# Optimization experiments

Hardware: AMD Instinct MI355X
Metric: run time of the kernel (lower is better)

## Reference

```python
import jax, jax.numpy as jnp
import numpy as np

EPS = 1e-5
DIL = 1
PAD = 1
STRIDE = 1

def conv2d(x, w, stride=1, pad=1, dil=1):
    return jax.lax.conv_general_dilated(x, w, (stride, stride), [(pad, pad), (pad, pad)],
                                        rhs_dilation=(dil, dil),
                                        dimension_numbers=('NCHW', 'OIHW', 'NCHW'))

def batchnorm(x, g, b, m, v):
    inv = g / jnp.sqrt(v + EPS)
    return x * inv[None, :, None, None] + (b - m * inv)[None, :, None, None]

def _bilinear(img, y, x):
    # img: [C,H,W]; y,x: [Ho,Wo] float sample coords; zero padding outside.
    H, W = img.shape[1], img.shape[2]
    y0 = jnp.floor(y); x0 = jnp.floor(x)
    ty = y - y0; tx = x - x0
    y0i = y0.astype(jnp.int32); x0i = x0.astype(jnp.int32)
    def g(yi, xi):
        valid = (yi >= 0) & (yi < H) & (xi >= 0) & (xi < W)
        v = img[:, jnp.clip(yi, 0, H - 1), jnp.clip(xi, 0, W - 1)]  # [C,Ho,Wo]
        return jnp.where(valid[None], v, jnp.zeros((), img.dtype))
    return (g(y0i, x0i) * ((1 - ty) * (1 - tx))[None]
            + g(y0i, x0i + 1) * ((1 - ty) * tx)[None]
            + g(y0i + 1, x0i) * (ty * (1 - tx))[None]
            + g(y0i + 1, x0i + 1) * (ty * tx)[None])

def deform_conv(x, w, offset, stride=1, pad=1, dil=1):
    # offset: [B, 18, Ho, Wo], channels 0:9 = dy per kernel tap (row-major), 9:18 = dx.
    B, C, H, W = x.shape
    Co = w.shape[0]
    Ho = (H + 2 * pad - dil * 2 - 1) // stride + 1
    Wo = (W + 2 * pad - dil * 2 - 1) // stride + 1
    off = offset.reshape(B, 2, 9, Ho, Wo)
    iy = (jnp.arange(Ho) * stride - pad).astype(x.dtype)
    ix = (jnp.arange(Wo) * stride - pad).astype(x.dtype)
    wk = w.reshape(Co, C, 9)
    out = jnp.zeros((B, Co, Ho, Wo), x.dtype)
    for k in range(9):  # fixed 3x3 kernel taps
        ky, kx = k // 3, k % 3
        ys = iy[:, None] + ky * dil + off[:, 0, k]  # [B,Ho,Wo]
        xs = ix[None, :] + kx * dil + off[:, 1, k]
        val = jax.vmap(_bilinear)(x, ys, xs)        # [B,C,Ho,Wo]
        out = out + jnp.einsum('bchw,oc->bohw', val, wk[:, :, k])
    return out

def offset_bias(dil, dtype):
    bw = jnp.array([[-1., 0., 1.]] * 3, dtype) * (dil - 1)
    bh = bw.T
    return jnp.concatenate([bh.reshape(-1), bw.reshape(-1)])  # [18]

def setup_inputs() -> dict:
    key = jax.random.key(0)
    ks = jax.random.split(key, 12)
    B, C, H, W = 8, 256, 56, 56
    inp = {
        'x': jax.random.normal(ks[0], (B, C, H, W), jnp.float32),
        'conv1_w': jax.random.normal(ks[1], (C, C, 3, 3), jnp.float32) * 0.02,
        'bn1_g': jax.random.normal(ks[2], (C,), jnp.float32) * 0.1 + 1.0,
        'bn1_b': jax.random.normal(ks[3], (C,), jnp.float32) * 0.1,
        'bn1_m': jax.random.normal(ks[4], (C,), jnp.float32) * 0.1,
        'bn1_v': jax.random.uniform(ks[5], (C,), jnp.float32) + 0.5,
        'off_w': jax.random.normal(ks[6], (18, C, 3, 3), jnp.float32) * 0.01,
        'off_b': jnp.zeros((18,), jnp.float32),
        'conv2_w': jax.random.normal(ks[7], (C, C, 3, 3), jnp.float32) * 0.02,
        'bn2_g': jax.random.normal(ks[8], (C,), jnp.float32) * 0.1 + 1.0,
        'bn2_b': jax.random.normal(ks[9], (C,), jnp.float32) * 0.1,
        'bn2_m': jax.random.normal(ks[10], (C,), jnp.float32) * 0.1,
        'bn2_v': jax.random.uniform(ks[11], (C,), jnp.float32) + 0.5,
    }
    return inp

def reference(x, conv1_w, bn1_g, bn1_b, bn1_m, bn1_v, off_w, off_b, conv2_w, bn2_g, bn2_b, bn2_m, bn2_v):
    residual = x
    out = conv2d(x, conv1_w, STRIDE, PAD, DIL)
    out = jax.nn.relu(batchnorm(out, bn1_g, bn1_b, bn1_m, bn1_v))
    offset = conv2d(out, off_w, STRIDE, PAD, DIL) + off_b[None, :, None, None]
    offset = offset + offset_bias(DIL, out.dtype)[None, :, None, None]
    out = deform_conv(out, conv2_w, offset, STRIDE, PAD, DIL)
    out = batchnorm(out, bn2_g, bn2_b, bn2_m, bn2_v)
    return jax.nn.relu(out + residual)
```

## Files before the change

kernel.cpp:

```cpp
#include <hip/hip_runtime.h>

#define NB 8
#define NH 56
#define NW 56
#define NHW 3136
#define NCHW 802816
#define NPIX 25088
#define NHP 58
#define EPSV 1e-5f
#define BUFS 20480

typedef float f32x4 __attribute__((ext_vector_type(4)));
typedef __bf16 bf16x8 __attribute__((ext_vector_type(8)));

__device__ __forceinline__ unsigned short f2b(float f) {
  unsigned int u = __float_as_uint(f);
  u += 0x7FFFu + ((u >> 16) & 1u);
  return (unsigned short)(u >> 16);
}
__device__ __forceinline__ float blo(unsigned int u){ return __uint_as_float(u << 16); }
__device__ __forceinline__ float bhi(unsigned int u){ return __uint_as_float(u & 0xFFFF0000u); }
__device__ __forceinline__ unsigned int pack_trunc(float f0, float f1) {
  return __builtin_amdgcn_perm(__float_as_uint(f1), __float_as_uint(f0), 0x07060302u);
}
__device__ __forceinline__ void soft_barrier() {
  __builtin_amdgcn_s_waitcnt(0xC07F);
  __builtin_amdgcn_s_barrier();
}

__global__ __launch_bounds__(256) void clear_borders(
    unsigned short* __restrict__ xbp, unsigned short* __restrict__ t1b)
{
  int i = blockIdx.x*256 + threadIdx.x;
  int q = i & 31; int pid = i >> 5;
  int b = pid / 228, j = pid % 228;
  int y, x;
  if (j < 58)       { y = 0;  x = j; }
  else if (j < 116) { y = 57; x = j - 58; }
  else { int jj = j - 116; y = 1 + (jj >> 1); x = (jj & 1) * 57; }
  size_t addr = ((size_t)(b*NHP + y)*NHP + x)*256 + q*8;
  uint4 z = make_uint4(0u,0u,0u,0u);
  *(uint4*)(xbp + addr) = z;
  *(uint4*)(t1b + addr) = z;
}

__global__ __launch_bounds__(256) void prep_x(
    const float* __restrict__ x, unsigned short* __restrict__ xbp)
{
  __shared__ float T[64][65];
  const int pxt  = blockIdx.x * 64;
  const int cg   = blockIdx.y * 64;
  const int b    = pxt / NHW;
  const int rem0 = pxt % NHW;
  const int t    = threadIdx.x;
  const int pl   = t & 63;
  const int c0   = t >> 6;
  const float* src = x + (size_t)b*NCHW + rem0;
  #pragma unroll
  for (int it = 0; it < 16; ++it) {
    int c = c0 + it*4;
    T[c][pl] = src[(size_t)(cg + c)*NHW + pl];
  }
  __syncthreads();
  const int pr = t >> 5;
  const int cp = t & 31;
  #pragma unroll
  for (int it = 0; it < 8; ++it) {
    int pxl = pr + it*8;
    int rem = rem0 + pxl;
    int ho = rem / NW, wo = rem % NW;
    unsigned int pk = ((unsigned int)f2b(T[cp*2+1][pxl]) << 16) | (unsigned int)f2b(T[cp*2][pxl]);
    *(unsigned int*)(xbp + ((size_t)(b*NHP + ho + 1)*NHP + (wo + 1))*256 + cg + cp*2) = pk;
  }
}

__global__ __launch_bounds__(256) void prep_w(
    const float* __restrict__ w, unsigned short* __restrict__ wp)
{
  int i = blockIdx.x*256 + threadIdx.x;
  int co = i / 2304;
  int r  = i % 2304;
  int k  = r >> 8;
  int ci = r & 255;
  wp[i] = f2b(w[((size_t)co*256 + ci)*9 + k]);
}

__global__ __launch_bounds__(256) void prep_w3(
    const float* __restrict__ ow, unsigned short* __restrict__ w3p)
{
  int i = blockIdx.x*256 + threadIdx.x;
  int co = i / 2304;
  int r  = i % 2304;
  int k  = r >> 8;
  int ci = r & 255;
  w3p[i] = (co < 18) ? f2b(ow[((size_t)co*256 + ci)*9 + k]) : (unsigned short)0;
}

__global__ __launch_bounds__(512, 4) void gemm_conv1(
    const unsigned short* __restrict__ xbp, const unsigned short* __restrict__ w1p,
    const float* __restrict__ gam, const float* __restrict__ bet,
    const float* __restrict__ mu,  const float* __restrict__ var,
    unsigned short* __restrict__ t1b)
{
  __shared__ unsigned short SMEM[2*BUFS];

  const int bx   = blockIdx.x;
  const int nbx  = (bx & 7)*49 + (bx >> 3);
  const int m0   = nbx * 64;
  const int t    = threadIdx.x;
  const int lane = t & 63;
  const int wv   = t >> 6;
  const int wvM  = wv & 1;
  const int wvN  = wv >> 1;
  const int quad = lane >> 4;
  const int l15  = lane & 15;

  const int srow = t >> 3;
  const int seg  = t & 7;
  const int sxor = srow & 7;
  const int px  = m0 + srow;
  const int b   = px / NHW, rem = px % NHW;
  const int ho  = rem / NW, wo = rem % NW;
  const unsigned int pbase = ((unsigned int)(b*NHP + ho)*NHP + wo)*256u + seg*8u;

  f32x4 acc[2][4];
  #pragma unroll
  for (int i = 0; i < 2; ++i)
    #pragma unroll
    for (int j = 0; j < 4; ++j) acc[i][j] = (f32x4)(0.f);

  uint4 pA, pB0, pB1, pB2, pB3;
  {
    pA  = *(const uint4*)(xbp + pbase);
    const unsigned int rb = seg*8u;
    pB0 = *(const uint4*)(w1p + (size_t)(srow      )*2304 + rb);
    pB1 = *(const uint4*)(w1p + (size_t)(srow +  64)*2304 + rb);
    pB2 = *(const uint4*)(w1p + (size_t)(srow + 128)*2304 + rb);
    pB3 = *(const uint4*)(w1p + (size_t)(srow + 192)*2304 + rb);
    *(uint4*)(&SMEM[srow*64 + ((seg ^ sxor)*8)]) = pA;
    *(uint4*)(&SMEM[4096 + (srow      )*64 + ((seg ^ sxor)*8)]) = pB0;
    *(uint4*)(&SMEM[4096 + (srow +  64)*64 + ((seg ^ sxor)*8)]) = pB1;
    *(uint4*)(&SMEM[4096 + (srow + 128)*64 + ((seg ^ sxor)*8)]) = pB2;
    *(uint4*)(&SMEM[4096 + (srow + 192)*64 + ((seg ^ sxor)*8)]) = pB3;
    pA  = *(const uint4*)(xbp + pbase + 64u);
    const unsigned int rb1 = 64u + seg*8u;
    pB0 = *(const uint4*)(w1p + (size_t)(srow      )*2304 + rb1);
    pB1 = *(const uint4*)(w1p + (size_t)(srow +  64)*2304 + rb1);
    pB2 = *(const uint4*)(w1p + (size_t)(srow + 128)*2304 + rb1);
    pB3 = *(const uint4*)(w1p + (size_t)(srow + 192)*2304 + rb1);
    soft_barrier();
  }

  for (int r = 0; r < 36; ++r) {
    unsigned short* Ac = SMEM + (r & 1)*BUFS;
    unsigned short* Bc = Ac + 4096;
    unsigned short* An = SMEM + ((r + 1) & 1)*BUFS;
    unsigned short* Bn = An + 4096;
    *(uint4*)(&An[srow*64 + ((seg ^ sxor)*8)]) = pA;
    *(uint4*)(&Bn[(srow      )*64 + ((seg ^ sxor)*8)]) = pB0;
    *(uint4*)(&Bn[(srow +  64)*64 + ((seg ^ sxor)*8)]) = pB1;
    *(uint4*)(&Bn[(srow + 128)*64 + ((seg ^ sxor)*8)]) = pB2;
    *(uint4*)(&Bn[(srow + 192)*64 + ((seg ^ sxor)*8)]) = pB3;
    {
      const int rn = (r < 34) ? r + 2 : 35;
      const int kn = rn >> 2, cicn = rn & 3;
      const int kyn = kn/3, kxn = kn - kyn*3;
      pA  = *(const uint4*)(xbp + pbase + (unsigned int)((kyn*NHP + kxn)*256 + cicn*64));
      const unsigned int rb = (unsigned int)(rn*64) + seg*8u;
      pB0 = *(const uint4*)(w1p + (size_t)(srow      )*2304 + rb);
      pB1 = *(const uint4*)(w1p + (size_t)(srow +  64)*2304 + rb);
      pB2 = *(const uint4*)(w1p + (size_t)(srow + 128)*2304 + rb);
      pB3 = *(const uint4*)(w1p + (size_t)(srow + 192)*2304 + rb);
    }
    #pragma unroll
    for (int kk = 0; kk < 2; ++kk) {
      const int s8 = (kk*4 + quad) ^ (l15 & 7);
      bf16x8 af[2], bfr[4];
      #pragma unroll
      for (int mt = 0; mt < 2; ++mt)
        af[mt] = *(const bf16x8*)(&Ac[(wvM*32 + mt*16 + l15)*64 + s8*8]);
      #pragma unroll
      for (int nt = 0; nt < 4; ++nt)
        bfr[nt] = *(const bf16x8*)(&Bc[(wvN*64 + nt*16 + l15)*64 + s8*8]);
      #pragma unroll
      for (int mt = 0; mt < 2; ++mt)
        #pragma unroll
        for (int nt = 0; nt < 4; ++nt)
          acc[mt][nt] = __builtin_amdgcn_mfma_f32_16x16x32_bf16(af[mt], bfr[nt], acc[mt][nt], 0, 0, 0);
    }
    soft_barrier();
  }

  __syncthreads();
  unsigned short* Sw = SMEM + wv*2304;
  #pragma unroll
  for (int nt = 0; nt < 4; ++nt) {
    const int co = wvN*64 + nt*16 + l15;
    const float inv  = gam[co] * rsqrtf(var[co] + EPSV);
    const float beta = bet[co] - mu[co]*inv;
    #pragma unroll
    for (int mt = 0; mt < 2; ++mt) {
      #pragma unroll
      for (int rr = 0; rr < 4; ++rr) {
        const int pxl = mt*16 + quad*4 + rr;
        float val = acc[mt][nt][rr]*inv + beta;
        val = val > 0.f ? val : 0.f;
        Sw[pxl*72 + nt*16 + l15] = f2b(val);
      }
    }
  }
  #pragma unroll
  for (int i = 0; i < 4; ++i) {
    const int pxl = (lane >> 3) + 8*i;
    const int sc  = lane & 7;
    uint4 q = *(const uint4*)(&Sw[pxl*72 + sc*8]);
    const int pg = m0 + wvM*32 + pxl;
    const int bb = pg / NHW, rm = pg % NHW;
    const int hh = rm / NW, ww = rm % NW;
    *(uint4*)(t1b + ((size_t)(bb*NHP + hh + 1)*NHP + ww + 1)*256 + wvN*64 + sc*8) = q;
  }
}

__global__ __launch_bounds__(256, 8) void gemm_off(
    const unsigned short* __restrict__ t1b, const unsigned short* __restrict__ w3p,
    const float* __restrict__ ob, float* __restrict__ toff)
{
  __shared__ unsigned short Al[4096];
  __shared__ unsigned short Bl[2048];

  const int bx  = blockIdx.x;
  const int nbx = (bx & 7)*49 + (bx >> 3);
  const int m0  = nbx * 64;
  const int kc = blockIdx.y;
  const int t    = threadIdx.x;
  const int lane = t & 63;
  const int wv   = t >> 6;
  const int quad = lane >> 4;
  const int l15  = lane & 15;

  const int arow = t >> 2;
  const int as4  = t & 3;
  const int axor = arow & 7;
  const int pxa  = m0 + arow;
  const int ba   = pxa / NHW, rema = pxa % NHW;
  const unsigned int pbase = ((unsigned int)(ba*NHP + rema/NW)*NHP + rema%NW)*256u;

  const int brow = t >> 3;
  const int bs   = t & 7;

  f32x4 acc[2];
  #pragma unroll
  for (int nt = 0; nt < 2; ++nt) {
    float init = 0.f;
    if (kc == 0) { int co = nt*16 + l15; init = (co < 18) ? ob[co] : 0.f; }
    acc[nt] = (f32x4)(init);
  }

  uint4 pA0, pA1, pB;
  {
    const int r = kc*9, k = r >> 2, cic = r & 3;
    const int ky = k/3, kx = k - ky*3;
    const unsigned int base = pbase + (unsigned int)((ky*NHP + kx)*256 + cic*64);
    pA0 = *(const uint4*)(t1b + base + as4*8);
    pA1 = *(const uint4*)(t1b + base + (as4+4)*8);
    pB  = *(const uint4*)(w3p + (size_t)brow*2304 + r*64 + bs*8);
  }

  for (int rr = 0; rr < 9; ++rr) {
    const int r = kc*9 + rr;
    __syncthreads();
    *(uint4*)(&Al[arow*64 + ((as4     ^ axor)*8)]) = pA0;
    *(uint4*)(&Al[arow*64 + (((as4+4) ^ axor)*8)]) = pA1;
    *(uint4*)(&Bl[brow*64 + ((bs ^ (brow & 7))*8)]) = pB;
    {
      const int rn = (rr < 8) ? r + 1 : r;
      const int kn = rn >> 2, cicn = rn & 3;
      const int kyn = kn/3, kxn = kn - kyn*3;
      const unsigned int base = pbase + (unsigned int)((kyn*NHP + kxn)*256 + cicn*64);
      pA0 = *(const uint4*)(t1b + base + as4*8);
      pA1 = *(const uint4*)(t1b + base + (as4+4)*8);
      pB  = *(const uint4*)(w3p + (size_t)brow*2304 + rn*64 + bs*8);
    }
    soft_barrier();
    #pragma unroll
    for (int kk = 0; kk < 2; ++kk) {
      const int s8 = (kk*4 + quad) ^ (l15 & 7);
      bf16x8 af = *(const bf16x8*)(&Al[(wv*16 + l15)*64 + s8*8]);
      #pragma unroll
      for (int nt = 0; nt < 2; ++nt) {
        bf16x8 bfr = *(const bf16x8*)(&Bl[(nt*16 + l15)*64 + s8*8]);
        acc[nt] = __builtin_amdgcn_mfma_f32_16x16x32_bf16(af, bfr, acc[nt], 0, 0, 0);
      }
    }
  }
  #pragma unroll
  for (int nt = 0; nt < 2; ++nt) {
    const int co = nt*16 + l15;
    if (co < 18) {
      #pragma unroll
      for (int rr2 = 0; rr2 < 4; ++rr2) {
        const int pg = m0 + wv*16 + quad*4 + rr2;
        const int bb = pg / NHW, rm = pg % NHW;
        atomicAdd(&toff[(size_t)bb*(18*NHW) + (size_t)co*NHW + rm], acc[nt][rr2]);
      }
    }
  }
}

__global__ __launch_bounds__(512, 4) void gemm_deform(
    const unsigned short* __restrict__ t1b, const unsigned short* __restrict__ w2p,
    const float* __restrict__ toff, const float* __restrict__ xres,
    const float* __restrict__ gam, const float* __restrict__ bet,
    const float* __restrict__ mu,  const float* __restrict__ var,
    float* __restrict__ outp)
{
  __shared__ unsigned short SMEM[2*BUFS];

  const int bid  = blockIdx.x;
  const int nb   = (bid & 7)*49 + (bid >> 3);
  const int m0   = nb * 64;
  const int t    = threadIdx.x;
  const int lane = t & 63;
  const int wv   = t >> 6;
  const int wvM  = wv & 1;
  const int wvN  = wv >> 1;
  const int quad = lane >> 4;
  const int l15  = lane & 15;

  const int srow = t >> 3;
  const int seg  = t & 7;
  const int sxor = srow & 7;
  const int px   = m0 + srow;
  const int b    = px / NHW, rem = px % NHW;
  const int ho   = rem / NW, wo = rem % NW;
  const int obb  = b*(18*NHW) + rem;
  const unsigned int prowb = (unsigned int)(b*NHP);

  f32x4 acc[2][4];
  #pragma unroll
  for (int i = 0; i < 2; ++i)
    #pragma unroll
    for (int j = 0; j < 4; ++j) acc[i][j] = (f32x4)(0.f);

  unsigned int o00, o01, o10, o11;
  float w00, w01, w10, w11;
#define COORDS(KK) {                                                   \
    const int ky_ = (KK)/3, kx_ = (KK) - ky_*3;                        \
    const float offy = toff[obb + (KK)*NHW];                           \
    const float offx = toff[obb + (9+(KK))*NHW];                       \
    const float yf = (float)(ho - 1 + ky_) + offy;                     \
    const float xf = (float)(wo - 1 + kx_) + offx;                     \
    const float y0f = floorf(yf), x0f = floorf(xf);                    \
    const float ty = yf - y0f,   tx = xf - x0f;                        \
    const int y0p = (int)y0f + 1, x0p = (int)x0f + 1;                  \
    const int cy0 = min(max(y0p,   0), NHP-1);                         \
    const int cy1 = min(max(y0p+1, 0), NHP-1);                         \
    const int cx0 = min(max(x0p,   0), NHP-1);                         \
    const int cx1 = min(max(x0p+1, 0), NHP-1);                         \
    w00 = (1.f-ty)*(1.f-tx);  w01 = (1.f-ty)*tx;                       \
    w10 = ty*(1.f-tx);        w11 = ty*tx;                             \
    o00 = ((prowb + cy0)*NHP + cx0)*256u + seg*8u;                     \
    o01 = ((prowb + cy0)*NHP + cx1)*256u + seg*8u;                     \
    o10 = ((prowb + cy1)*NHP + cx0)*256u + seg*8u;                     \
    o11 = ((prowb + cy1)*NHP + cx1)*256u + seg*8u;                     \
  }

#define PACK_WRITE(DST) {                                                        \
    uint4 res;                                                                   \
    { float a0 = w00*blo(pc00.x) + w01*blo(pc01.x) + w10*blo(pc10.x) + w11*blo(pc11.x); \
      float a1 = w00*bhi(pc00.x) + w01*bhi(pc01.x) + w10*bhi(pc10.x) + w11*bhi(pc11.x); \
      res.x = pack_trunc(a0, a1); }                                              \
    { float a0 = w00*blo(pc00.y) + w01*blo(pc01.y) + w10*blo(pc10.y) + w11*blo(pc11.y); \
      float a1 = w00*bhi(pc00.y) + w01*bhi(pc01.y) + w10*bhi(pc10.y) + w11*bhi(pc11.y); \
      res.y = pack_trunc(a0, a1); }                                              \
    { float a0 = w00*blo(pc00.z) + w01*blo(pc01.z) + w10*blo(pc10.z) + w11*blo(pc11.z); \
      float a1 = w00*bhi(pc00.z) + w01*bhi(pc01.z) + w10*bhi(pc10.z) + w11*bhi(pc11.z); \
      res.z = pack_trunc(a0, a1); }                                              \
    { float a0 = w00*blo(pc00.w) + w01*blo(pc01.w) + w10*blo(pc10.w) + w11*blo(pc11.w); \
      float a1 = w00*bhi(pc00.w) + w01*bhi(pc01.w) + w10*bhi(pc10.w) + w11*bhi(pc11.w); \
      res.w = pack_trunc(a0, a1); }                                              \
    *(uint4*)(&(DST)[srow*64 + ((seg ^ sxor)*8)]) = res;                         \
  }

  COORDS(0);
  uint4 pc00, pc01, pc10, pc11, pB0, pB1, pB2, pB3;
  {
    pc00 = *(const uint4*)(t1b + o00);
    pc01 = *(const uint4*)(t1b + o01);
    pc10 = *(const uint4*)(t1b + o10);
    pc11 = *(const uint4*)(t1b + o11);
    const unsigned int rb = seg*8u;
    pB0 = *(const uint4*)(w2p + (size_t)(srow      )*2304 + rb);
    pB1 = *(const uint4*)(w2p + (size_t)(srow +  64)*2304 + rb);
    pB2 = *(const uint4*)(w2p + (size_t)(srow + 128)*2304 + rb);
    pB3 = *(const uint4*)(w2p + (size_t)(srow + 192)*2304 + rb);
    PACK_WRITE(SMEM);
    *(uint4*)(&SMEM[4096 + (srow      )*64 + ((seg ^ sxor)*8)]) = pB0;
    *(uint4*)(&SMEM[4096 + (srow +  64)*64 + ((seg ^ sxor)*8)]) = pB1;
    *(uint4*)(&SMEM[4096 + (srow + 128)*64 + ((seg ^ sxor)*8)]) = pB2;
    *(uint4*)(&SMEM[4096 + (srow + 192)*64 + ((seg ^ sxor)*8)]) = pB3;
    pc00 = *(const uint4*)(t1b + o00 + 64u);
    pc01 = *(const uint4*)(t1b + o01 + 64u);
    pc10 = *(const uint4*)(t1b + o10 + 64u);
    pc11 = *(const uint4*)(t1b + o11 + 64u);
    const unsigned int rb1 = 64u + seg*8u;
    pB0 = *(const uint4*)(w2p + (size_t)(srow      )*2304 + rb1);
    pB1 = *(const uint4*)(w2p + (size_t)(srow +  64)*2304 + rb1);
    pB2 = *(const uint4*)(w2p + (size_t)(srow + 128)*2304 + rb1);
    pB3 = *(const uint4*)(w2p + (size_t)(srow + 192)*2304 + rb1);
    soft_barrier();
  }

  for (int r = 0; r < 36; ++r) {
    unsigned short* Ac = SMEM + (r & 1)*BUFS;
    unsigned short* Bc = Ac + 4096;
    unsigned short* An = SMEM + ((r + 1) & 1)*BUFS;
    unsigned short* Bn = An + 4096;
    PACK_WRITE(An);
    *(uint4*)(&Bn[(srow      )*64 + ((seg ^ sxor)*8)]) = pB0;
    *(uint4*)(&Bn[(srow +  64)*64 + ((seg ^ sxor)*8)]) = pB1;
    *(uint4*)(&Bn[(srow + 128)*64 + ((seg ^ sxor)*8)]) = pB2;
    *(uint4*)(&Bn[(srow + 192)*64 + ((seg ^ sxor)*8)]) = pB3;
    if ((r & 3) == 2 && r < 34) COORDS((r + 2) >> 2);
    {
      const int rn = (r < 34) ? r + 2 : 35;
      const unsigned int cio = (unsigned int)((rn & 3)*64);
      pc00 = *(const uint4*)(t1b + o00 + cio);
      pc01 = *(const uint4*)(t1b + o01 + cio);
      pc10 = *(const uint4*)(t1b + o10 + cio);
      pc11 = *(const uint4*)(t1b + o11 + cio);
      const unsigned int rb = (unsigned int)(rn*64) + seg*8u;
      pB0 = *(const uint4*)(w2p + (size_t)(srow      )*2304 + rb);
      pB1 = *(const uint4*)(w2p + (size_t)(srow +  64)*2304 + rb);
      pB2 = *(const uint4*)(w2p + (size_t)(srow + 128)*2304 + rb);
      pB3 = *(const uint4*)(w2p + (size_t)(srow + 192)*2304 + rb);
    }
    #pragma unroll
    for (int kk = 0; kk < 2; ++kk) {
      const int s8 = (kk*4 + quad) ^ (l15 & 7);
      bf16x8 af[2], bfr[4];
      #pragma unroll
      for (int mt = 0; mt < 2; ++mt)
        af[mt] = *(const bf16x8*)(&Ac[(wvM*32 + mt*16 + l15)*64 + s8*8]);
      #pragma unroll
      for (int nt = 0; nt < 4; ++nt)
        bfr[nt] = *(const bf16x8*)(&Bc[(wvN*64 + nt*16 + l15)*64 + s8*8]);
      #pragma unroll
      for (int mt = 0; mt < 2; ++mt)
        #pragma unroll
        for (int nt = 0; nt < 4; ++nt)
          acc[mt][nt] = __builtin_amdgcn_mfma_f32_16x16x32_bf16(af[mt], bfr[nt], acc[mt][nt], 0, 0, 0);
    }
    soft_barrier();
  }
#undef COORDS
#undef PACK_WRITE

  __syncthreads();
  float* Sl = (float*)SMEM + wv*1056;
  const int pxl_r = lane & 31;
  const int csel  = lane >> 5;
  const int pg    = m0 + wvM*32 + pxl_r;
  const int bo    = pg / NHW, remo = pg % NHW;
  const size_t obase = (size_t)bo*NCHW + remo;
  #pragma unroll
  for (int h = 0; h < 2; ++h) {
    #pragma unroll
    for (int nt2 = 0; nt2 < 2; ++nt2) {
      const int nt = h*2 + nt2;
      #pragma unroll
      for (int mt = 0; mt < 2; ++mt) {
        #pragma unroll
        for (int rr = 0; rr < 4; ++rr) {
          const int pxl = mt*16 + quad*4 + rr;
          Sl[pxl*33 + nt2*16 + l15] = acc[mt][nt][rr];
        }
      }
    }
    #pragma unroll
    for (int j = 0; j < 16; ++j) {
      const int col = csel*16 + j;
      const int co  = wvN*64 + h*32 + col;
      const float inv  = gam[co] * rsqrtf(var[co] + EPSV);
      const float beta = bet[co] - mu[co]*inv;
      const size_t off = obase + (size_t)co*NHW;
      float val = Sl[pxl_r*33 + col];
      float o = val*inv + beta + xres[off];
      outp[off] = o > 0.f ? o : 0.f;
    }
  }
}

extern "C" void kernel_launch(void* const* d_in, const int* in_sizes, int n_in,
                              void* d_out, int out_size, void* d_ws, size_t ws_size,
                              hipStream_t stream) {
  const float* x   = (const float*)d_in[0];
  const float* w1  = (const float*)d_in[1];
  const float* g1  = (const float*)d_in[2];
  const float* b1  = (const float*)d_in[3];
  const float* m1  = (const float*)d_in[4];
  const float* v1  = (const float*)d_in[5];
  const float* ow  = (const float*)d_in[6];
  const float* ob  = (const float*)d_in[7];
  const float* w2  = (const float*)d_in[8];
  const float* g2  = (const float*)d_in[9];
  const float* b2  = (const float*)d_in[10];
  const float* m2  = (const float*)d_in[11];
  const float* v2  = (const float*)d_in[12];
  float* out = (float*)d_out;

  const size_t PADSZ = (size_t)NB*NHP*NHP*256;
  unsigned short* xbp = (unsigned short*)d_ws;
  unsigned short* t1b = xbp + PADSZ;
  float*          tof = (float*)(t1b + PADSZ);
  unsigned short* w1p = (unsigned short*)(tof + (size_t)NB*18*NHW);
  unsigned short* w2p = w1p + (size_t)589824;
  unsigned short* w3p = w2p + (size_t)589824;

  clear_borders<<<228, 256, 0, stream>>>(xbp, t1b);
  dim3 gp(392, 4, 1);
  prep_x<<<gp, 256, 0, stream>>>(x, xbp);
  prep_w<<<2304, 256, 0, stream>>>(w1, w1p);
  prep_w<<<2304, 256, 0, stream>>>(w2, w2p);
  prep_w3<<<288, 256, 0, stream>>>(ow, w3p);
  hipMemsetAsync(tof, 0, (size_t)NB*18*NHW*sizeof(float), stream);

  gemm_conv1<<<392, 512, 0, stream>>>(xbp, w1p, g1, b1, m1, v1, t1b);
  dim3 go(392, 4, 1);
  gemm_off<<<go, 256, 0, stream>>>(t1b, w3p, ob, tof);
  gemm_deform<<<392, 512, 0, stream>>>(t1b, w2p, tof, x, g2, b2, m2, v2, out);
}
```

Measured before the change: 250.7 us.

## Deepen register prefetch to three stages and move LDS stores after MFMA

Both GEMM main loops (conv1 and the deformable conv2) now keep two sets of prefetch registers and issue global loads three rounds ahead instead of two. The loop is unrolled by two so the register sets alternate. The shared-memory stores for the next round are moved to after the MFMA block, so global-load latency has more time to hide behind compute. In the deformable loop the bilinear weights are snapshotted per stage and COORDS is computed one round earlier. The cost is higher register pressure, which may reduce occupancy or cause spills.

```diff
diff --git a/kernel.cpp b/kernel.cpp
--- a/kernel.cpp
+++ b/kernel.cpp
@@ -129,67 +129,71 @@
     #pragma unroll
     for (int j = 0; j < 4; ++j) acc[i][j] = (f32x4)(0.f);
 
-  uint4 pA, pB0, pB1, pB2, pB3;
+  uint4 saA, saB0, saB1, saB2, saB3;
+  uint4 sbA, sbB0, sbB1, sbB2, sbB3;
+
+#define C1_ISSUE(SA_, SB0_, SB1_, SB2_, SB3_, RN) {                       \
+    const int kn_ = (RN) >> 2, cicn_ = (RN) & 3;                          \
+    const int kyn_ = kn_/3, kxn_ = kn_ - kyn_*3;                          \
+    SA_  = *(const uint4*)(xbp + pbase + (unsigned int)((kyn_*NHP + kxn_)*256 + cicn_*64)); \
+    const unsigned int rb_ = (unsigned int)((RN)*64) + seg*8u;            \
+    SB0_ = *(const uint4*)(w1p + (size_t)(srow      )*2304 + rb_);        \
+    SB1_ = *(const uint4*)(w1p + (size_t)(srow +  64)*2304 + rb_);        \
+    SB2_ = *(const uint4*)(w1p + (size_t)(srow + 128)*2304 + rb_);        \
+    SB3_ = *(const uint4*)(w1p + (size_t)(srow + 192)*2304 + rb_);        \
+  }
+
   {
-    pA  = *(const uint4*)(xbp + pbase);
-    const unsigned int rb = seg*8u;
-    pB0 = *(const uint4*)(w1p + (size_t)(srow      )*2304 + rb);
-    pB1 = *(const uint4*)(w1p + (size_t)(srow +  64)*2304 + rb);
-    pB2 = *(const uint4*)(w1p + (size_t)(srow + 128)*2304 + rb);
-    pB3 = *(const uint4*)(w1p + (size_t)(srow + 192)*2304 + rb);
-    *(uint4*)(&SMEM[srow*64 + ((seg ^ sxor)*8)]) = pA;
-    *(uint4*)(&SMEM[4096 + (srow      )*64 + ((seg ^ sxor)*8)]) = pB0;
-    *(uint4*)(&SMEM[4096 + (srow +  64)*64 + ((seg ^ sxor)*8)]) = pB1;
-    *(uint4*)(&SMEM[4096 + (srow + 128)*64 + ((seg ^ sxor)*8)]) = pB2;
-    *(uint4*)(&SMEM[4096 + (srow + 192)*64 + ((seg ^ sxor)*8)]) = pB3;
-    pA  = *(const uint4*)(xbp + pbase + 64u);
-    const unsigned int rb1 = 64u + seg*8u;
-    pB0 = *(const uint4*)(w1p + (size_t)(srow      )*2304 + rb1);
-    pB1 = *(const uint4*)(w1p + (size_t)(srow +  64)*2304 + rb1);
-    pB2 = *(const uint4*)(w1p + (size_t)(srow + 128)*2304 + rb1);
-    pB3 = *(const uint4*)(w1p + (size_t)(srow + 192)*2304 + rb1);
+    uint4 tA, tB0, tB1, tB2, tB3;
+    C1_ISSUE(tA, tB0, tB1, tB2, tB3, 0);
+    *(uint4*)(&SMEM[srow*64 + ((seg ^ sxor)*8)]) = tA;
+    *(uint4*)(&SMEM[4096 + (srow      )*64 + ((seg ^ sxor)*8)]) = tB0;
+    *(uint4*)(&SMEM[4096 + (srow +  64)*64 + ((seg ^ sxor)*8)]) = tB1;
+    *(uint4*)(&SMEM[4096 + (srow + 128)*64 + ((seg ^ sxor)*8)]) = tB2;
+    *(uint4*)(&SMEM[4096 + (srow + 192)*64 + ((seg ^ sxor)*8)]) = tB3;
+    C1_ISSUE(sbA, sbB0, sbB1, sbB2, sbB3, 1);
+    C1_ISSUE(saA, saB0, saB1, saB2, saB3, 2);
     soft_barrier();
   }
 
-  for (int r = 0; r < 36; ++r) {
-    unsigned short* Ac = SMEM + (r & 1)*BUFS;
-    unsigned short* Bc = Ac + 4096;
-    unsigned short* An = SMEM + ((r + 1) & 1)*BUFS;
-    unsigned short* Bn = An + 4096;
-    *(uint4*)(&An[srow*64 + ((seg ^ sxor)*8)]) = pA;
-    *(uint4*)(&Bn[(srow      )*64 + ((seg ^ sxor)*8)]) = pB0;
-    *(uint4*)(&Bn[(srow +  64)*64 + ((seg ^ sxor)*8)]) = pB1;
-    *(uint4*)(&Bn[(srow + 128)*64 + ((seg ^ sxor)*8)]) = pB2;
-    *(uint4*)(&Bn[(srow + 192)*64 + ((seg ^ sxor)*8)]) = pB3;
-    {
-      const int rn = (r < 34) ? r + 2 : 35;
-      const int kn = rn >> 2, cicn = rn & 3;
-      const int kyn = kn/3, kxn = kn - kyn*3;
-      pA  = *(const uint4*)(xbp + pbase + (unsigned int)((kyn*NHP + kxn)*256 + cicn*64));
-      const unsigned int rb = (unsigned int)(rn*64) + seg*8u;
-      pB0 = *(const uint4*)(w1p + (size_t)(srow      )*2304 + rb);
-      pB1 = *(const uint4*)(w1p + (size_t)(srow +  64)*2304 + rb);
-      pB2 = *(const uint4*)(w1p + (size_t)(srow + 128)*2304 + rb);
-      pB3 = *(const uint4*)(w1p + (size_t)(srow + 192)*2304 + rb);
-    }
-    #pragma unroll
-    for (int kk = 0; kk < 2; ++kk) {
-      const int s8 = (kk*4 + quad) ^ (l15 & 7);
-      bf16x8 af[2], bfr[4];
-      #pragma unroll
-      for (int mt = 0; mt < 2; ++mt)
-        af[mt] = *(const bf16x8*)(&Ac[(wvM*32 + mt*16 + l15)*64 + s8*8]);
-      #pragma unroll
-      for (int nt = 0; nt < 4; ++nt)
-        bfr[nt] = *(const bf16x8*)(&Bc[(wvN*64 + nt*16 + l15)*64 + s8*8]);
-      #pragma unroll
-      for (int mt = 0; mt < 2; ++mt)
-        #pragma unroll
-        for (int nt = 0; nt < 4; ++nt)
-          acc[mt][nt] = __builtin_amdgcn_mfma_f32_16x16x32_bf16(af[mt], bfr[nt], acc[mt][nt], 0, 0, 0);
-    }
-    soft_barrier();
-  }
+#define C1_ROUND(R, SA_, SB0_, SB1_, SB2_, SB3_) {                        \
+    const int r_ = (R);                                                   \
+    unsigned short* Ac = SMEM + (r_ & 1)*BUFS;                            \
+    unsigned short* Bc = Ac + 4096;                                       \
+    unsigned short* An = SMEM + ((r_ + 1) & 1)*BUFS;                      \
+    unsigned short* Bn = An + 4096;                                       \
+    _Pragma("unroll")                                                     \
+    for (int kk = 0; kk < 2; ++kk) {                                      \
+      const int s8 = (kk*4 + quad) ^ (l15 & 7);                           \
+      bf16x8 af[2], bfr[4];                                               \
+      _Pragma("unroll")                                                   \
+      for (int mt = 0; mt < 2; ++mt)                                      \
+        af[mt] = *(const bf16x8*)(&Ac[(wvM*32 + mt*16 + l15)*64 + s8*8]); \
+      _Pragma("unroll")                                                   \
+      for (int nt = 0; nt < 4; ++nt)                                      \
+        bfr[nt] = *(const bf16x8*)(&Bc[(wvN*64 + nt*16 + l15)*64 + s8*8]);\
+      _Pragma("unroll")                                                   \
+      for (int mt = 0; mt < 2; ++mt)                                      \
+        _Pragma("unroll")                                                 \
+        for (int nt = 0; nt < 4; ++nt)                                    \
+          acc[mt][nt] = __builtin_amdgcn_mfma_f32_16x16x32_bf16(af[mt], bfr[nt], acc[mt][nt], 0, 0, 0); \
+    }                                                                     \
+    *(uint4*)(&An[srow*64 + ((seg ^ sxor)*8)]) = SA_;                     \
+    *(uint4*)(&Bn[(srow      )*64 + ((seg ^ sxor)*8)]) = SB0_;            \
+    *(uint4*)(&Bn[(srow +  64)*64 + ((seg ^ sxor)*8)]) = SB1_;            \
+    *(uint4*)(&Bn[(srow + 128)*64 + ((seg ^ sxor)*8)]) = SB2_;            \
+    *(uint4*)(&Bn[(srow + 192)*64 + ((seg ^ sxor)*8)]) = SB3_;            \
+    const int rn_ = (r_ < 33) ? r_ + 3 : 35;                              \
+    C1_ISSUE(SA_, SB0_, SB1_, SB2_, SB3_, rn_);                           \
+    soft_barrier();                                                       \
+  }
+
+  for (int r = 0; r < 36; r += 2) {
+    C1_ROUND(r,     sbA, sbB0, sbB1, sbB2, sbB3);
+    C1_ROUND(r + 1, saA, saB0, saB1, saB2, saB3);
+  }
+#undef C1_ROUND
+#undef C1_ISSUE
 
   __syncthreads();
   unsigned short* Sw = SMEM + wv*2304;
@@ -365,96 +369,107 @@
     o11 = ((prowb + cy1)*NHP + cx1)*256u + seg*8u;                     \
   }
 
-#define PACK_WRITE(DST) {                                                        \
-    uint4 res;                                                                   \
-    { float a0 = w00*blo(pc00.x) + w01*blo(pc01.x) + w10*blo(pc10.x) + w11*blo(pc11.x); \
-      float a1 = w00*bhi(pc00.x) + w01*bhi(pc01.x) + w10*bhi(pc10.x) + w11*bhi(pc11.x); \
-      res.x = pack_trunc(a0, a1); }                                              \
-    { float a0 = w00*blo(pc00.y) + w01*blo(pc01.y) + w10*blo(pc10.y) + w11*blo(pc11.y); \
-      float a1 = w00*bhi(pc00.y) + w01*bhi(pc01.y) + w10*bhi(pc10.y) + w11*bhi(pc11.y); \
-      res.y = pack_trunc(a0, a1); }                                              \
-    { float a0 = w00*blo(pc00.z) + w01*blo(pc01.z) + w10*blo(pc10.z) + w11*blo(pc11.z); \
-      float a1 = w00*bhi(pc00.z) + w01*bhi(pc01.z) + w10*bhi(pc10.z) + w11*bhi(pc11.z); \
-      res.z = pack_trunc(a0, a1); }                                              \
-    { float a0 = w00*blo(pc00.w) + w01*blo(pc01.w) + w10*blo(pc10.w) + w11*blo(pc11.w); \
-      float a1 = w00*bhi(pc00.w) + w01*bhi(pc01.w) + w10*bhi(pc10.w) + w11*bhi(pc11.w); \
-      res.w = pack_trunc(a0, a1); }                                              \
-    *(uint4*)(&(DST)[srow*64 + ((seg ^ sxor)*8)]) = res;                         \
-  }
+#define PACKW(C00,C01,C10,C11,W00,W01,W10,W11,DST) {                            \
+    uint4 res;                                                                  \
+    { float a0 = W00*blo(C00.x) + W01*blo(C01.x) + W10*blo(C10.x) + W11*blo(C11.x); \
+      float a1 = W00*bhi(C00.x) + W01*bhi(C01.x) + W10*bhi(C10.x) + W11*bhi(C11.x); \
+      res.x = pack_trunc(a0, a1); }                                             \
+    { float a0 = W00*blo(C00.y) + W01*blo(C01.y) + W10*blo(C10.y) + W11*blo(C11.y); \
+      float a1 = W00*bhi(C00.y) + W01*bhi(C01.y) + W10*bhi(C10.y) + W11*bhi(C11.y); \
+      res.y = pack_trunc(a0, a1); }                                             \
+    { float a0 = W00*blo(C00.z) + W01*blo(C01.z) + W10*blo(C10.z) + W11*blo(C11.z); \
+      float a1 = W00*bhi(C00.z) + W01*bhi(C01.z) + W10*bhi(C10.z) + W11*bhi(C11.z); \
+      res.z = pack_trunc(a0, a1); }                                             \
+    { float a0 = W00*blo(C00.w) + W01*blo(C01.w) + W10*blo(C10.w) + W11*blo(C11.w); \
+      float a1 = W00*bhi(C00.w) + W01*bhi(C01.w) + W10*bhi(C10.w) + W11*bhi(C11.w); \
+      res.w = pack_trunc(a0, a1); }                                             \
+    *(uint4*)(&(DST)[srow*64 + ((seg ^ sxor)*8)]) = res;                        \
+  }
+
+#define ISSUEC(C00,C01,C10,C11,W00,W01,W10,W11,RN) {                            \
+    const unsigned int cio_ = (unsigned int)(((RN) & 3)*64);                    \
+    C00 = *(const uint4*)(t1b + o00 + cio_);                                    \
+    C01 = *(const uint4*)(t1b + o01 + cio_);                                    \
+    C10 = *(const uint4*)(t1b + o10 + cio_);                                    \
+    C11 = *(const uint4*)(t1b + o11 + cio_);                                    \
+    W00 = w00; W01 = w01; W10 = w10; W11 = w11;                                 \
+  }
+
+#define ISSUEB(RN) {                                                            \
+    const unsigned int rb_ = (unsigned int)((RN)*64) + seg*8u;                  \
+    pB0 = *(const uint4*)(w2p + (size_t)(srow      )*2304 + rb_);               \
+    pB1 = *(const uint4*)(w2p + (size_t)(srow +  64)*2304 + rb_);               \
+    pB2 = *(const uint4*)(w2p + (size_t)(srow + 128)*2304 + rb_);               \
+    pB3 = *(const uint4*)(w2p + (size_t)(srow + 192)*2304 + rb_);               \
+  }
+
+  uint4 ca00, ca01, ca10, ca11, cb00, cb01, cb10, cb11;
+  float cwa00, cwa01, cwa10, cwa11, cwb00, cwb01, cwb10, cwb11;
+  uint4 pB0, pB1, pB2, pB3;
 
   COORDS(0);
-  uint4 pc00, pc01, pc10, pc11, pB0, pB1, pB2, pB3;
   {
-    pc00 = *(const uint4*)(t1b + o00);
-    pc01 = *(const uint4*)(t1b + o01);
-    pc10 = *(const uint4*)(t1b + o10);
-    pc11 = *(const uint4*)(t1b + o11);
-    const unsigned int rb = seg*8u;
-    pB0 = *(const uint4*)(w2p + (size_t)(srow      )*2304 + rb);
-    pB1 = *(const uint4*)(w2p + (size_t)(srow +  64)*2304 + rb);
-    pB2 = *(const uint4*)(w2p + (size_t)(srow + 128)*2304 + rb);
-    pB3 = *(const uint4*)(w2p + (size_t)(srow + 192)*2304 + rb);
-    PACK_WRITE(SMEM);
+    uint4 t00, t01, t10, t11;
+    t00 = *(const uint4*)(t1b + o00);
+    t01 = *(const uint4*)(t1b + o01);
+    t10 = *(const uint4*)(t1b + o10);
+    t11 = *(const uint4*)(t1b + o11);
+    ISSUEB(0);
+    PACKW(t00, t01, t10, t11, w00, w01, w10, w11, SMEM);
     *(uint4*)(&SMEM[4096 + (srow      )*64 + ((seg ^ sxor)*8)]) = pB0;
     *(uint4*)(&SMEM[4096 + (srow +  64)*64 + ((seg ^ sxor)*8)]) = pB1;
     *(uint4*)(&SMEM[4096 + (srow + 128)*64 + ((seg ^ sxor)*8)]) = pB2;
     *(uint4*)(&SMEM[4096 + (srow + 192)*64 + ((seg ^ sxor)*8)]) = pB3;
-    pc00 = *(const uint4*)(t1b + o00 + 64u);
-    pc01 = *(const uint4*)(t1b + o01 + 64u);
-    pc10 = *(const uint4*)(t1b + o10 + 64u);
-    pc11 = *(const uint4*)(t1b + o11 + 64u);
-    const unsigned int rb1 = 64u + seg*8u;
-    pB0 = *(const uint4*)(w2p + (size_t)(srow      )*2304 + rb1);
-    pB1 = *(const uint4*)(w2p + (size_t)(srow +  64)*2304 + rb1);
-    pB2 = *(const uint4*)(w2p + (size_t)(srow + 128)*2304 + rb1);
-    pB3 = *(const uint4*)(w2p + (size_t)(srow + 192)*2304 + rb1);
+    ISSUEC(cb00, cb01, cb10, cb11, cwb00, cwb01, cwb10, cwb11, 1);
+    ISSUEB(1);
+    ISSUEC(ca00, ca01, ca10, ca11, cwa00, cwa01, cwa10, cwa11, 2);
     soft_barrier();
   }
 
-  for (int r = 0; r < 36; ++r) {
-    unsigned short* Ac = SMEM + (r & 1)*BUFS;
-    unsigned short* Bc = Ac + 4096;
-    unsigned short* An = SMEM + ((r + 1) & 1)*BUFS;
-    unsigned short* Bn = An + 4096;
-    PACK_WRITE(An);
-    *(uint4*)(&Bn[(srow      )*64 + ((seg ^ sxor)*8)]) = pB0;
-    *(uint4*)(&Bn[(srow +  64)*64 + ((seg ^ sxor)*8)]) = pB1;
-    *(uint4*)(&Bn[(srow + 128)*64 + ((seg ^ sxor)*8)]) = pB2;
-    *(uint4*)(&Bn[(srow + 192)*64 + ((seg ^ sxor)*8)]) = pB3;
-    if ((r & 3) == 2 && r < 34) COORDS((r + 2) >> 2);
-    {
-      const int rn = (r < 34) ? r + 2 : 35;
-      const unsigned int cio = (unsigned int)((rn & 3)*64);
-      pc00 = *(const uint4*)(t1b + o00 + cio);
-      pc01 = *(const uint4*)(t1b + o01 + cio);
-      pc10 = *(const uint4*)(t1b + o10 + cio);
-      pc11 = *(const uint4*)(t1b + o11 + cio);
-      const unsigned int rb = (unsigned int)(rn*64) + seg*8u;
-      pB0 = *(const uint4*)(w2p + (size_t)(srow      )*2304 + rb);
-      pB1 = *(const uint4*)(w2p + (size_t)(srow +  64)*2304 + rb);
-      pB2 = *(const uint4*)(w2p + (size_t)(srow + 128)*2304 + rb);
-      pB3 = *(const uint4*)(w2p + (size_t)(srow + 192)*2304 + rb);
-    }
-    #pragma unroll
-    for (int kk = 0; kk < 2; ++kk) {
-      const int s8 = (kk*4 + quad) ^ (l15 & 7);
-      bf16x8 af[2], bfr[4];
-      #pragma unroll
-      for (int mt = 0; mt < 2; ++mt)
-        af[mt] = *(const bf16x8*)(&Ac[(wvM*32 + mt*16 + l15)*64 + s8*8]);
-      #pragma unroll
-      for (int nt = 0; nt < 4; ++nt)
-        bfr[nt] = *(const bf16x8*)(&Bc[(wvN*64 + nt*16 + l15)*64 + s8*8]);
-      #pragma unroll
-      for (int mt = 0; mt < 2; ++mt)
-        #pragma unroll
-        for (int nt = 0; nt < 4; ++nt)
-          acc[mt][nt] = __builtin_amdgcn_mfma_f32_16x16x32_bf16(af[mt], bfr[nt], acc[mt][nt], 0, 0, 0);
-    }
-    soft_barrier();
-  }
+#define DROUND(R, C00,C01,C10,C11, W00,W01,W10,W11) {                           \
+    const int r_ = (R);                                                         \
+    unsigned short* Ac = SMEM + (r_ & 1)*BUFS;                                  \
+    unsigned short* Bc = Ac + 4096;                                             \
+    unsigned short* An = SMEM + ((r_ + 1) & 1)*BUFS;                            \
+    unsigned short* Bn = An + 4096;                                             \
+    if ((r_ & 3) == 1 && r_ < 33) COORDS((r_ + 3) >> 2);                        \
+    _Pragma("unroll")                                                           \
+    for (int kk = 0; kk < 2; ++kk) {                                            \
+      const int s8 = (kk*4 + quad) ^ (l15 & 7);                                 \
+      bf16x8 af[2], bfr[4];                                                     \
+      _Pragma("unroll")                                                         \
+      for (int mt = 0; mt < 2; ++mt)                                            \
+        af[mt] = *(const bf16x8*)(&Ac[(wvM*32 + mt*16 + l15)*64 + s8*8]);       \
+      _Pragma("unroll")                                                         \
+      for (int nt = 0; nt < 4; ++nt)                                            \
+        bfr[nt] = *(const bf16x8*)(&Bc[(wvN*64 + nt*16 + l15)*64 + s8*8]);      \
+      _Pragma("unroll")                                                         \
+      for (int mt = 0; mt < 2; ++mt)                                            \
+        _Pragma("unroll")                                                       \
+        for (int nt = 0; nt < 4; ++nt)                                          \
+          acc[mt][nt] = __builtin_amdgcn_mfma_f32_16x16x32_bf16(af[mt], bfr[nt], acc[mt][nt], 0, 0, 0); \
+    }                                                                           \
+    PACKW(C00, C01, C10, C11, W00, W01, W10, W11, An);                          \
+    *(uint4*)(&Bn[(srow      )*64 + ((seg ^ sxor)*8)]) = pB0;                   \
+    *(uint4*)(&Bn[(srow +  64)*64 + ((seg ^ sxor)*8)]) = pB1;                   \
+    *(uint4*)(&Bn[(srow + 128)*64 + ((seg ^ sxor)*8)]) = pB2;                   \
+    *(uint4*)(&Bn[(srow + 192)*64 + ((seg ^ sxor)*8)]) = pB3;                   \
+    const int rnB_ = (r_ < 34) ? r_ + 2 : 35;                                   \
+    ISSUEB(rnB_);                                                               \
+    const int rn3_ = (r_ < 33) ? r_ + 3 : 35;                                   \
+    ISSUEC(C00, C01, C10, C11, W00, W01, W10, W11, rn3_);                       \
+    soft_barrier();                                                             \
+  }
+
+  for (int r = 0; r < 36; r += 2) {
+    DROUND(r,     cb00, cb01, cb10, cb11, cwb00, cwb01, cwb10, cwb11);
+    DROUND(r + 1, ca00, ca01, ca10, ca11, cwa00, cwa01, cwa10, cwa11);
+  }
+#undef DROUND
+#undef ISSUEB
+#undef ISSUEC
+#undef PACKW
 #undef COORDS
-#undef PACK_WRITE
 
   __syncthreads();
   float* Sl = (float*)SMEM + wv*1056;
```

New measurement: 281.9 us. +12.4%, slower.

## Use direct global-to-LDS loads in conv GEMMs and merge prep launches

Applied to the files above, without the earlier changes.

Replaces the register-staged global loads and LDS stores for the A/B tiles in gemm_conv1, and for the weight tiles in gemm_deform, with global_load_lds DMA. This shortens prefetch distance to one stage and swaps the soft barrier for __syncthreads. It also folds the three weight-prep kernels into one launch and moves the offset-buffer memset into clear_borders. The intent is to cut VGPR pressure, LDS store instructions and launch overhead. The risk is that the shorter prefetch exposes memory latency, and the swizzle mapping for the DMA layout must match the existing reads.

```diff
diff --git a/kernel.cpp b/kernel.cpp
--- a/kernel.cpp
+++ b/kernel.cpp
@@ -9,6 +9,7 @@
 #define NHP 58
 #define EPSV 1e-5f
 #define BUFS 20480
+#define TOFN 451584
 
 typedef float f32x4 __attribute__((ext_vector_type(4)));
 typedef __bf16 bf16x8 __attribute__((ext_vector_type(8)));
@@ -27,9 +28,16 @@
   __builtin_amdgcn_s_waitcnt(0xC07F);
   __builtin_amdgcn_s_barrier();
 }
+__device__ __forceinline__ void dma16(const unsigned short* g, unsigned short* l) {
+  __builtin_amdgcn_global_load_lds(
+      (const __attribute__((address_space(1))) unsigned int*)g,
+      (__attribute__((address_space(3))) unsigned int*)l,
+      16, 0, 0);
+}
 
 __global__ __launch_bounds__(256) void clear_borders(
-    unsigned short* __restrict__ xbp, unsigned short* __restrict__ t1b)
+    unsigned short* __restrict__ xbp, unsigned short* __restrict__ t1b,
+    float* __restrict__ tof)
 {
   int i = blockIdx.x*256 + threadIdx.x;
   int q = i & 31; int pid = i >> 5;
@@ -42,6 +50,11 @@
   uint4 z = make_uint4(0u,0u,0u,0u);
   *(uint4*)(xbp + addr) = z;
   *(uint4*)(t1b + addr) = z;
+  int zi = i*8;
+  if (zi < TOFN) {
+    *(float4*)(tof + zi)     = make_float4(0.f,0.f,0.f,0.f);
+    *(float4*)(tof + zi + 4) = make_float4(0.f,0.f,0.f,0.f);
+  }
 }
 
 __global__ __launch_bounds__(256) void prep_x(
@@ -74,26 +87,25 @@
   }
 }
 
-__global__ __launch_bounds__(256) void prep_w(
-    const float* __restrict__ w, unsigned short* __restrict__ wp)
+__global__ __launch_bounds__(256) void prep_w_all(
+    const float* __restrict__ w1, const float* __restrict__ w2,
+    const float* __restrict__ ow,
+    unsigned short* __restrict__ w1p, unsigned short* __restrict__ w2p,
+    unsigned short* __restrict__ w3p)
 {
   int i = blockIdx.x*256 + threadIdx.x;
-  int co = i / 2304;
-  int r  = i % 2304;
-  int k  = r >> 8;
-  int ci = r & 255;
-  wp[i] = f2b(w[((size_t)co*256 + ci)*9 + k]);
-}
-
-__global__ __launch_bounds__(256) void prep_w3(
-    const float* __restrict__ ow, unsigned short* __restrict__ w3p)
-{
-  int i = blockIdx.x*256 + threadIdx.x;
-  int co = i / 2304;
-  int r  = i % 2304;
-  int k  = r >> 8;
-  int ci = r & 255;
-  w3p[i] = (co < 18) ? f2b(ow[((size_t)co*256 + ci)*9 + k]) : (unsigned short)0;
+  if (i < 589824) {
+    int co = i / 2304, r = i % 2304, k = r >> 8, ci = r & 255;
+    w1p[i] = f2b(w1[((size_t)co*256 + ci)*9 + k]);
+  } else if (i < 1179648) {
+    int j = i - 589824;
+    int co = j / 2304, r = j % 2304, k = r >> 8, ci = r & 255;
+    w2p[j] = f2b(w2[((size_t)co*256 + ci)*9 + k]);
+  } else {
+    int j = i - 1179648;
+    int co = j / 2304, r = j % 2304, k = r >> 8, ci = r & 255;
+    w3p[j] = (co < 18) ? f2b(ow[((size_t)co*256 + ci)*9 + k]) : (unsigned short)0;
+  }
 }
 
 __global__ __launch_bounds__(512, 4) void gemm_conv1(
@@ -117,11 +129,14 @@
 
   const int srow = t >> 3;
   const int seg  = t & 7;
-  const int sxor = srow & 7;
+  const int swz8 = ((seg ^ (srow & 7))*8);
   const int px  = m0 + srow;
   const int b   = px / NHW, rem = px % NHW;
   const int ho  = rem / NW, wo = rem % NW;
-  const unsigned int pbase = ((unsigned int)(b*NHP + ho)*NHP + wo)*256u + seg*8u;
+  const unsigned int pbaseA = ((unsigned int)(b*NHP + ho)*NHP + wo)*256u + (unsigned int)swz8;
+  const int rowB0 = wv*32 + (lane >> 3);
+  const unsigned int bswz = (unsigned int)(((lane & 7) ^ (lane >> 3))*8);
+  const int chA = wv*512;
 
   f32x4 acc[2][4];
   #pragma unroll
@@ -129,26 +144,12 @@
     #pragma unroll
     for (int j = 0; j < 4; ++j) acc[i][j] = (f32x4)(0.f);
 
-  uint4 pA, pB0, pB1, pB2, pB3;
   {
-    pA  = *(const uint4*)(xbp + pbase);
-    const unsigned int rb = seg*8u;
-    pB0 = *(const uint4*)(w1p + (size_t)(srow      )*2304 + rb);
-    pB1 = *(const uint4*)(w1p + (size_t)(srow +  64)*2304 + rb);
-    pB2 = *(const uint4*)(w1p + (size_t)(srow + 128)*2304 + rb);
-    pB3 = *(const uint4*)(w1p + (size_t)(srow + 192)*2304 + rb);
-    *(uint4*)(&SMEM[srow*64 + ((seg ^ sxor)*8)]) = pA;
-    *(uint4*)(&SMEM[4096 + (srow      )*64 + ((seg ^ sxor)*8)]) = pB0;
-    *(uint4*)(&SMEM[4096 + (srow +  64)*64 + ((seg ^ sxor)*8)]) = pB1;
-    *(uint4*)(&SMEM[4096 + (srow + 128)*64 + ((seg ^ sxor)*8)]) = pB2;
-    *(uint4*)(&SMEM[4096 + (srow + 192)*64 + ((seg ^ sxor)*8)]) = pB3;
-    pA  = *(const uint4*)(xbp + pbase + 64u);
-    const unsigned int rb1 = 64u + seg*8u;
-    pB0 = *(const uint4*)(w1p + (size_t)(srow      )*2304 + rb1);
-    pB1 = *(const uint4*)(w1p + (size_t)(srow +  64)*2304 + rb1);
-    pB2 = *(const uint4*)(w1p + (size_t)(srow + 128)*2304 + rb1);
-    pB3 = *(const uint4*)(w1p + (size_t)(srow + 192)*2304 + rb1);
-    soft_barrier();
+    dma16(xbp + pbaseA, &SMEM[chA]);
+    #pragma unroll
+    for (int j = 0; j < 4; ++j)
+      dma16(w1p + (size_t)(rowB0 + j*8)*2304 + bswz, &SMEM[4096 + (wv*4 + j)*512]);
+    __syncthreads();
   }
 
   for (int r = 0; r < 36; ++r) {
@@ -156,21 +157,16 @@
     unsigned short* Bc = Ac + 4096;
     unsigned short* An = SMEM + ((r + 1) & 1)*BUFS;
     unsigned short* Bn = An + 4096;
-    *(uint4*)(&An[srow*64 + ((seg ^ sxor)*8)]) = pA;
-    *(uint4*)(&Bn[(srow      )*64 + ((seg ^ sxor)*8)]) = pB0;
-    *(uint4*)(&Bn[(srow +  64)*64 + ((seg ^ sxor)*8)]) = pB1;
-    *(uint4*)(&Bn[(srow + 128)*64 + ((seg ^ sxor)*8)]) = pB2;
-    *(uint4*)(&Bn[(srow + 192)*64 + ((seg ^ sxor)*8)]) = pB3;
     {
-      const int rn = (r < 34) ? r + 2 : 35;
+      const int rn = (r < 35) ? r + 1 : 35;
       const int kn = rn >> 2, cicn = rn & 3;
       const int kyn = kn/3, kxn = kn - kyn*3;
-      pA  = *(const uint4*)(xbp + pbase + (unsigned int)((kyn*NHP + kxn)*256 + cicn*64));
-      const unsigned int rb = (unsigned int)(rn*64) + seg*8u;
-      pB0 = *(const uint4*)(w1p + (size_t)(srow      )*2304 + rb);
-      pB1 = *(const uint4*)(w1p + (size_t)(srow +  64)*2304 + rb);
-      pB2 = *(const uint4*)(w1p + (size_t)(srow + 128)*2304 + rb);
-      pB3 = *(const uint4*)(w1p + (size_t)(srow + 192)*2304 + rb);
+      const unsigned int koff = (unsigned int)((kyn*NHP + kxn)*256 + cicn*64);
+      dma16(xbp + pbaseA + koff, &An[chA]);
+      const unsigned int rb = (unsigned int)(rn*64);
+      #pragma unroll
+      for (int j = 0; j < 4; ++j)
+        dma16(w1p + (size_t)(rowB0 + j*8)*2304 + rb + bswz, &Bn[(wv*4 + j)*512]);
     }
     #pragma unroll
     for (int kk = 0; kk < 2; ++kk) {
@@ -188,10 +184,9 @@
         for (int nt = 0; nt < 4; ++nt)
           acc[mt][nt] = __builtin_amdgcn_mfma_f32_16x16x32_bf16(af[mt], bfr[nt], acc[mt][nt], 0, 0, 0);
     }
-    soft_barrier();
-  }
-
-  __syncthreads();
+    __syncthreads();
+  }
+
   unsigned short* Sw = SMEM + wv*2304;
   #pragma unroll
   for (int nt = 0; nt < 4; ++nt) {
@@ -335,6 +330,9 @@
   const int ho   = rem / NW, wo = rem % NW;
   const int obb  = b*(18*NHW) + rem;
   const unsigned int prowb = (unsigned int)(b*NHP);
+
+  const int rowB0 = wv*32 + (lane >> 3);
+  const unsigned int bswz = (unsigned int)(((lane & 7) ^ (lane >> 3))*8);
 
   f32x4 acc[2][4];
   #pragma unroll
@@ -365,50 +363,42 @@
     o11 = ((prowb + cy1)*NHP + cx1)*256u + seg*8u;                     \
   }
 
-#define PACK_WRITE(DST) {                                                        \
-    uint4 res;                                                                   \
+#define PACKW(DST) {                                                            \
+    uint4 res;                                                                  \
     { float a0 = w00*blo(pc00.x) + w01*blo(pc01.x) + w10*blo(pc10.x) + w11*blo(pc11.x); \
       float a1 = w00*bhi(pc00.x) + w01*bhi(pc01.x) + w10*bhi(pc10.x) + w11*bhi(pc11.x); \
-      res.x = pack_trunc(a0, a1); }                                              \
+      res.x = pack_trunc(a0, a1); }                                             \
     { float a0 = w00*blo(pc00.y) + w01*blo(pc01.y) + w10*blo(pc10.y) + w11*blo(pc11.y); \
       float a1 = w00*bhi(pc00.y) + w01*bhi(pc01.y) + w10*bhi(pc10.y) + w11*bhi(pc11.y); \
-      res.y = pack_trunc(a0, a1); }                                              \
+      res.y = pack_trunc(a0, a1); }                                             \
     { float a0 = w00*blo(pc00.z) + w01*blo(pc01.z) + w10*blo(pc10.z) + w11*blo(pc11.z); \
       float a1 = w00*bhi(pc00.z) + w01*bhi(pc01.z) + w10*bhi(pc10.z) + w11*bhi(pc11.z); \
-      res.z = pack_trunc(a0, a1); }                                              \
+      res.z = pack_trunc(a0, a1); }                                             \
     { float a0 = w00*blo(pc00.w) + w01*blo(pc01.w) + w10*blo(pc10.w) + w11*blo(pc11.w); \
       float a1 = w00*bhi(pc00.w) + w01*bhi(pc01.w) + w10*bhi(pc10.w) + w11*bhi(pc11.w); \
-      res.w = pack_trunc(a0, a1); }                                              \
-    *(uint4*)(&(DST)[srow*64 + ((seg ^ sxor)*8)]) = res;                         \
-  }
+      res.w = pack_trunc(a0, a1); }                                             \
+    *(uint4*)(&(DST)[srow*64 + ((seg ^ sxor)*8)]) = res;                        \
+  }
+
+#define ISSUEC(RN) {                                                           \
+    const unsigned int cio_ = (unsigned int)(((RN) & 3)*64);                   \
+    pc00 = *(const uint4*)(t1b + o00 + cio_);                                  \
+    pc01 = *(const uint4*)(t1b + o01 + cio_);                                  \
+    pc10 = *(const uint4*)(t1b + o10 + cio_);                                  \
+    pc11 = *(const uint4*)(t1b + o11 + cio_);                                  \
+  }
+
+  uint4 pc00, pc01, pc10, pc11;
 
   COORDS(0);
-  uint4 pc00, pc01, pc10, pc11, pB0, pB1, pB2, pB3;
   {
-    pc00 = *(const uint4*)(t1b + o00);
-    pc01 = *(const uint4*)(t1b + o01);
-    pc10 = *(const uint4*)(t1b + o10);
-    pc11 = *(const uint4*)(t1b + o11);
-    const unsigned int rb = seg*8u;
-    pB0 = *(const uint4*)(w2p + (size_t)(srow      )*2304 + rb);
-    pB1 = *(const uint4*)(w2p + (size_t)(srow +  64)*2304 + rb);
-    pB2 = *(const uint4*)(w2p + (size_t)(srow + 128)*2304 + rb);
-    pB3 = *(const uint4*)(w2p + (size_t)(srow + 192)*2304 + rb);
-    PACK_WRITE(SMEM);
-    *(uint4*)(&SMEM[4096 + (srow      )*64 + ((seg ^ sxor)*8)]) = pB0;
-    *(uint4*)(&SMEM[4096 + (srow +  64)*64 + ((seg ^ sxor)*8)]) = pB1;
-    *(uint4*)(&SMEM[4096 + (srow + 128)*64 + ((seg ^ sxor)*8)]) = pB2;
-    *(uint4*)(&SMEM[4096 + (srow + 192)*64 + ((seg ^ sxor)*8)]) = pB3;
-    pc00 = *(const uint4*)(t1b + o00 + 64u);
-    pc01 = *(const uint4*)(t1b + o01 + 64u);
-    pc10 = *(const uint4*)(t1b + o10 + 64u);
-    pc11 = *(const uint4*)(t1b + o11 + 64u);
-    const unsigned int rb1 = 64u + seg*8u;
-    pB0 = *(const uint4*)(w2p + (size_t)(srow      )*2304 + rb1);
-    pB1 = *(const uint4*)(w2p + (size_t)(srow +  64)*2304 + rb1);
-    pB2 = *(const uint4*)(w2p + (size_t)(srow + 128)*2304 + rb1);
-    pB3 = *(const uint4*)(w2p + (size_t)(srow + 192)*2304 + rb1);
-    soft_barrier();
+    ISSUEC(0);
+    #pragma unroll
+    for (int j = 0; j < 4; ++j)
+      dma16(w2p + (size_t)(rowB0 + j*8)*2304 + bswz, &SMEM[4096 + (wv*4 + j)*512]);
+    PACKW(SMEM);
+    ISSUEC(1);
+    __syncthreads();
   }
 
   for (int r = 0; r < 36; ++r) {
@@ -416,24 +406,18 @@
     unsigned short* Bc = Ac + 4096;
     unsigned short* An = SMEM + ((r + 1) & 1)*BUFS;
     unsigned short* Bn = An + 4096;
-    PACK_WRITE(An);
-    *(uint4*)(&Bn[(srow      )*64 + ((seg ^ sxor)*8)]) = pB0;
-    *(uint4*)(&Bn[(srow +  64)*64 + ((seg ^ sxor)*8)]) = pB1;
-    *(uint4*)(&Bn[(srow + 128)*64 + ((seg ^ sxor)*8)]) = pB2;
-    *(uint4*)(&Bn[(srow + 192)*64 + ((seg ^ sxor)*8)]) = pB3;
+    PACKW(An);
+    {
+      const int rnB = (r < 35) ? r + 1 : 35;
+      const unsigned int rb = (unsigned int)(rnB*64);
+      #pragma unroll
+      for (int j = 0; j < 4; ++j)
+        dma16(w2p + (size_t)(rowB0 + j*8)*2304 + rb + bswz, &Bn[(wv*4 + j)*512]);
+    }
     if ((r & 3) == 2 && r < 34) COORDS((r + 2) >> 2);
     {
       const int rn = (r < 34) ? r + 2 : 35;
-      const unsigned int cio = (unsigned int)((rn & 3)*64);
-      pc00 = *(const uint4*)(t1b + o00 + cio);
-      pc01 = *(const uint4*)(t1b + o01 + cio);
-      pc10 = *(const uint4*)(t1b + o10 + cio);
-      pc11 = *(const uint4*)(t1b + o11 + cio);
-      const unsigned int rb = (unsigned int)(rn*64) + seg*8u;
-      pB0 = *(const uint4*)(w2p + (size_t)(srow      )*2304 + rb);
-      pB1 = *(const uint4*)(w2p + (size_t)(srow +  64)*2304 + rb);
-      pB2 = *(const uint4*)(w2p + (size_t)(srow + 128)*2304 + rb);
-      pB3 = *(const uint4*)(w2p + (size_t)(srow + 192)*2304 + rb);
+      ISSUEC(rn);
     }
     #pragma unroll
     for (int kk = 0; kk < 2; ++kk) {
@@ -451,12 +435,12 @@
         for (int nt = 0; nt < 4; ++nt)
           acc[mt][nt] = __builtin_amdgcn_mfma_f32_16x16x32_bf16(af[mt], bfr[nt], acc[mt][nt], 0, 0, 0);
     }
-    soft_barrier();
-  }
+    __syncthreads();
+  }
+#undef ISSUEC
+#undef PACKW
 #undef COORDS
-#undef PACK_WRITE
-
-  __syncthreads();
+
   float* Sl = (float*)SMEM + wv*1056;
   const int pxl_r = lane & 31;
   const int csel  = lane >> 5;
@@ -517,13 +501,10 @@
   unsigned short* w2p = w1p + (size_t)589824;
   unsigned short* w3p = w2p + (size_t)589824;
 
-  clear_borders<<<228, 256, 0, stream>>>(xbp, t1b);
+  clear_borders<<<228, 256, 0, stream>>>(xbp, t1b, tof);
   dim3 gp(392, 4, 1);
   prep_x<<<gp, 256, 0, stream>>>(x, xbp);
-  prep_w<<<2304, 256, 0, stream>>>(w1, w1p);
-  prep_w<<<2304, 256, 0, stream>>>(w2, w2p);
-  prep_w3<<<288, 256, 0, stream>>>(ow, w3p);
-  hipMemsetAsync(tof, 0, (size_t)NB*18*NHW*sizeof(float), stream);
+  prep_w_all<<<4896, 256, 0, stream>>>(w1, w2, ow, w1p, w2p, w3p);
 
   gemm_conv1<<<392, 512, 0, stream>>>(xbp, w1p, g1, b1, m1, v1, t1b);
   dim3 go(392, 4, 1);
```

Measured after the change: 235.3 us. 1.07x faster.
